# Performance work log

Hardware: AMD Instinct MI355X
Metric: run time of the kernel (lower is better)

The kernel has to match this reference:

```python
import jax, jax.numpy as jnp
import numpy as np
from math import sqrt

EMBED_DIM = 1024
PROJ_DIM = 128
BATCH = 4
SEQ = 4096


def setup_inputs() -> dict:
    key = jax.random.key(0)
    ks = jax.random.split(key, 7)
    x = jax.random.normal(ks[0], (BATCH, SEQ, EMBED_DIM), dtype=jnp.float32)
    # nn.Linear default init scale ~ 1/sqrt(fan_in); use small random weights
    s_e = 1.0 / sqrt(EMBED_DIM)
    Wq = jax.random.uniform(ks[1], (EMBED_DIM, PROJ_DIM), jnp.float32, -s_e, s_e)
    bq = jax.random.uniform(ks[2], (PROJ_DIM,), jnp.float32, -s_e, s_e)
    Wk = jax.random.uniform(ks[3], (EMBED_DIM, PROJ_DIM), jnp.float32, -s_e, s_e)
    bk = jax.random.uniform(ks[4], (PROJ_DIM,), jnp.float32, -s_e, s_e)
    Wov = jax.random.uniform(ks[5], (EMBED_DIM, EMBED_DIM), jnp.float32, -s_e, s_e)
    bov = jax.random.uniform(ks[6], (EMBED_DIM,), jnp.float32, -s_e, s_e)
    return {"x": x, "Wq": Wq, "bq": bq, "Wk": Wk, "bk": bk, "Wov": Wov, "bov": bov}


def reference(x, Wq, bq, Wk, bk, Wov, bov):
    # q, k: (b, s, p); ov: (b, s, d)
    queries = jnp.einsum('bse,ep->bsp', x, Wq) + bq
    keys = jnp.einsum('bse,ep->bsp', x, Wk) + bk
    scores = jnp.einsum('bqp,bkp->bqk', queries, keys) / sqrt(PROJ_DIM)
    pattern = jax.nn.softmax(scores, axis=-1)
    ov = jnp.einsum('bse,ed->bsd', x, Wov) + bov
    return jnp.einsum('bqk,bkd->bqd', pattern, ov)
```

## Files before the change

kernel.cpp:

```cpp
#include <hip/hip_runtime.h>
#include <hip/hip_bf16.h>

#define BATCH 4
#define SEQ   4096
#define EMB   1024
#define PDIM  128

using short8   = __attribute__((ext_vector_type(8))) short;
using ushort8  = __attribute__((ext_vector_type(8))) unsigned short;
using float4v  = __attribute__((ext_vector_type(4))) float;

__device__ __forceinline__ unsigned short f2bf(float f) {
  union { float f; unsigned int u; } x; x.f = f;
  unsigned int r = x.u + 0x7fffu + ((x.u >> 16) & 1u);
  return (unsigned short)(r >> 16);
}

__device__ __forceinline__ void gld_lds16(const unsigned short* g, unsigned short* l) {
  __builtin_amdgcn_global_load_lds(
      (__attribute__((address_space(1))) void*)(g),
      (__attribute__((address_space(3))) void*)(l), 16, 0, 0);
}

__global__ void xprep_kernel(const float* __restrict__ src,
                             unsigned short* __restrict__ rm,
                             unsigned short* __restrict__ tp, int R, int C) {
  __shared__ float tile[32][33];
  const float* s = src + (size_t)blockIdx.z * R * C;
  unsigned short* drm = rm + (size_t)blockIdx.z * R * C;
  unsigned short* dtp = tp + (size_t)blockIdx.z * R * C;
  int c0 = blockIdx.x * 32, r0 = blockIdx.y * 32;
#pragma unroll
  for (int i = 0; i < 32; i += 8) {
    float v = s[(size_t)(r0 + threadIdx.y + i) * C + c0 + threadIdx.x];
    tile[threadIdx.y + i][threadIdx.x] = v;
    drm[(size_t)(r0 + threadIdx.y + i) * C + c0 + threadIdx.x] = f2bf(v);
  }
  __syncthreads();
#pragma unroll
  for (int i = 0; i < 32; i += 8)
    dtp[(size_t)(c0 + threadIdx.y + i) * R + r0 + threadIdx.x] =
        f2bf(tile[threadIdx.x][threadIdx.y + i]);
}

__global__ void transpose_cast_kernel(const float* __restrict__ src,
                                      unsigned short* __restrict__ dst, int R, int C) {
  __shared__ float tile[32][33];
  int c0 = blockIdx.x * 32, r0 = blockIdx.y * 32;
#pragma unroll
  for (int i = 0; i < 32; i += 8)
    tile[threadIdx.y + i][threadIdx.x] =
        src[(size_t)(r0 + threadIdx.y + i) * C + c0 + threadIdx.x];
  __syncthreads();
#pragma unroll
  for (int i = 0; i < 32; i += 8)
    dst[(size_t)(c0 + threadIdx.y + i) * R + r0 + threadIdx.x] =
        f2bf(tile[threadIdx.x][threadIdx.y + i]);
}

__global__ void concat_bias_kernel(const float* __restrict__ a,
                                   const float* __restrict__ b,
                                   float* __restrict__ o) {
  int i = threadIdx.x;
  o[i] = (i < PDIM) ? a[i] : b[i - PDIM];
}

template <int NT>
__global__ __launch_bounds__(256, 2) void gemm_kernel(
    const unsigned short* __restrict__ A, int lda, size_t saz,
    const unsigned short* __restrict__ Bt, int ldb, size_t sbz,
    void* __restrict__ Cv, int ldc, size_t scz,
    int K, const float* __restrict__ bias,
    float* __restrict__ lsum, int slz,
    float scale, int mode) {
  constexpr int NW = NT / 32;
  constexpr int BC = NT / 64;
  __shared__ __attribute__((aligned(16))) unsigned short As[128 * 32];
  __shared__ __attribute__((aligned(16))) unsigned short Bs[NT * 32];
  const int tid = threadIdx.x;
  const int wave = tid >> 6, lane = tid & 63;
  const int quad = lane >> 4, l16 = lane & 15;
  const int m0 = blockIdx.x * 128, n0 = blockIdx.y * NT;
  const int z = blockIdx.z;
  const int mq = (wave >> 1) * 64, nq = (wave & 1) * (NT / 2);

  A  += (size_t)z * saz;
  Bt += (size_t)z * sbz;

  const int lr = lane >> 2;
  const int koff = (((lane & 3) ^ ((lane >> 3) & 3)) << 3);
  const unsigned short* Ag[2];
  unsigned short* Al[2];
#pragma unroll
  for (int j = 0; j < 2; j++) {
    int c = wave * 2 + j;
    Ag[j] = A + (size_t)(m0 + c * 16 + lr) * lda + koff;
    Al[j] = As + c * 512;
  }
  const unsigned short* Bg[BC];
  unsigned short* Bl[BC];
#pragma unroll
  for (int j = 0; j < BC; j++) {
    int c = wave * BC + j;
    Bg[j] = Bt + (size_t)(n0 + c * 16 + lr) * ldb + koff;
    Bl[j] = Bs + c * 512;
  }

  float4v zf = {0.f, 0.f, 0.f, 0.f};
  float4v acc[4][NW];
#pragma unroll
  for (int i = 0; i < 4; i++)
#pragma unroll
    for (int j = 0; j < NW; j++) acc[i][j] = zf;

  const int rsw = ((l16 >> 1) & 3);

  for (int k0 = 0; k0 < K; k0 += 32) {
    if (k0) __syncthreads();
#pragma unroll
    for (int j = 0; j < 2; j++) gld_lds16(Ag[j] + k0, Al[j]);
#pragma unroll
    for (int j = 0; j < BC; j++) gld_lds16(Bg[j] + k0, Bl[j]);
    __syncthreads();

    short8 af[4], bfr[NW];
#pragma unroll
    for (int t = 0; t < 4; t++)
      af[t] = *(const short8*)(As + (mq + t * 16 + l16) * 32 + ((quad ^ rsw) << 3));
#pragma unroll
    for (int t = 0; t < NW; t++)
      bfr[t] = *(const short8*)(Bs + (nq + t * 16 + l16) * 32 + ((quad ^ rsw) << 3));
#pragma unroll
    for (int mt = 0; mt < 4; mt++)
#pragma unroll
      for (int nt = 0; nt < NW; nt++)
        acc[mt][nt] = __builtin_amdgcn_mfma_f32_16x16x32_bf16(af[mt], bfr[nt], acc[mt][nt], 0, 0, 0);
  }

  float* Cf = (float*)Cv + (size_t)z * scz;
  unsigned short* Cb = (unsigned short*)Cv + (size_t)z * scz;

  if (mode == 1) {
    float rsum[4][4];
#pragma unroll
    for (int mt = 0; mt < 4; mt++)
#pragma unroll
      for (int r = 0; r < 4; r++) rsum[mt][r] = 0.f;
#pragma unroll
    for (int mt = 0; mt < 4; mt++)
#pragma unroll
      for (int nt = 0; nt < NW; nt++) {
        int gn = n0 + nq + nt * 16 + l16;
#pragma unroll
        for (int r = 0; r < 4; r++) {
          float e = __expf(acc[mt][nt][r] * scale);
          Cb[(size_t)(m0 + mq + mt * 16 + quad * 4 + r) * ldc + gn] = f2bf(e);
          rsum[mt][r] += e;
        }
      }
#pragma unroll
    for (int mt = 0; mt < 4; mt++)
#pragma unroll
      for (int r = 0; r < 4; r++) {
        float s = rsum[mt][r];
#pragma unroll
        for (int o = 1; o < 16; o <<= 1) s += __shfl_xor(s, o);
        rsum[mt][r] = s;
      }
    if (l16 == 0) {
#pragma unroll
      for (int mt = 0; mt < 4; mt++)
#pragma unroll
        for (int r = 0; r < 4; r++)
          atomicAdd(&lsum[(size_t)z * slz + m0 + mq + mt * 16 + quad * 4 + r], rsum[mt][r]);
    }
  } else if (mode == 2) {
    float linv[4][4];
#pragma unroll
    for (int mt = 0; mt < 4; mt++)
#pragma unroll
      for (int r = 0; r < 4; r++)
        linv[mt][r] = 1.f / lsum[(size_t)z * slz + m0 + mq + mt * 16 + quad * 4 + r];
#pragma unroll
    for (int mt = 0; mt < 4; mt++)
#pragma unroll
      for (int nt = 0; nt < NW; nt++) {
        int gn = n0 + nq + nt * 16 + l16;
#pragma unroll
        for (int r = 0; r < 4; r++)
          Cb[(size_t)(m0 + mq + mt * 16 + quad * 4 + r) * ldc + gn] =
              f2bf(acc[mt][nt][r] * linv[mt][r]);
      }
  } else {
#pragma unroll
    for (int mt = 0; mt < 4; mt++)
#pragma unroll
      for (int nt = 0; nt < NW; nt++) {
        int gn = n0 + nq + nt * 16 + l16;
        float bv = bias[gn];
#pragma unroll
        for (int r = 0; r < 4; r++) {
          int gm = m0 + mq + mt * 16 + quad * 4 + r;
          float v = acc[mt][nt][r] + bv;
          if (mode == 0) Cf[(size_t)gm * ldc + gn] = v;
          else           Cb[(size_t)gm * ldc + gn] = f2bf(v);
        }
      }
  }
}

extern "C" void kernel_launch(void* const* d_in, const int* in_sizes, int n_in,
                              void* d_out, int out_size, void* d_ws, size_t ws_size,
                              hipStream_t stream) {
  const float* x   = (const float*)d_in[0];
  const float* Wq  = (const float*)d_in[1];
  const float* bq  = (const float*)d_in[2];
  const float* Wk  = (const float*)d_in[3];
  const float* bk  = (const float*)d_in[4];
  const float* Wov = (const float*)d_in[5];
  const float* bov = (const float*)d_in[6];
  float* out = (float*)d_out;

  char* ws = (char*)d_ws;
  size_t off = 0;
  auto alloc = [&](size_t bytes) {
    char* p = ws + off;
    off += (bytes + 255) & ~(size_t)255;
    return p;
  };
  const int M = BATCH * SEQ;
  unsigned short* x_bf = (unsigned short*)alloc((size_t)M * EMB * 2);
  unsigned short* xT   = (unsigned short*)alloc((size_t)M * EMB * 2);
  unsigned short* WqkT = (unsigned short*)alloc((size_t)2 * PDIM * EMB * 2);
  unsigned short* WovT = (unsigned short*)alloc((size_t)EMB * EMB * 2);
  float*          bqk  = (float*)alloc(2 * PDIM * sizeof(float));
  unsigned short* qk   = (unsigned short*)alloc((size_t)M * 2 * PDIM * 2);
  float*          linv = (float*)alloc((size_t)M * sizeof(float));
  unsigned short* ctx  = (unsigned short*)alloc((size_t)M * EMB * 2);
  const size_t pslot = (size_t)SEQ * SEQ * 2;
  unsigned short* P = (unsigned short*)(ws + off);
  size_t rem = ws_size > off ? ws_size - off : 0;
  int g = (rem >= 4 * pslot) ? 4 : (rem >= 2 * pslot) ? 2 : 1;

  xprep_kernel<<<dim3(EMB / 32, SEQ / 32, BATCH), dim3(32, 8), 0, stream>>>(x, x_bf, xT, SEQ, EMB);
  transpose_cast_kernel<<<dim3(PDIM / 32, EMB / 32), dim3(32, 8), 0, stream>>>(Wq, WqkT, EMB, PDIM);
  transpose_cast_kernel<<<dim3(PDIM / 32, EMB / 32), dim3(32, 8), 0, stream>>>(Wk, WqkT + (size_t)PDIM * EMB, EMB, PDIM);
  transpose_cast_kernel<<<dim3(EMB / 32, EMB / 32), dim3(32, 8), 0, stream>>>(Wov, WovT, EMB, EMB);
  concat_bias_kernel<<<1, 256, 0, stream>>>(bq, bk, bqk);
  hipMemsetAsync(linv, 0, M * sizeof(float), stream);

  gemm_kernel<128><<<dim3(M / 128, 2, 1), 256, 0, stream>>>(
      x_bf, EMB, 0, WqkT, EMB, 0, qk, 2 * PDIM, 0, EMB, bqk, nullptr, 0, 1.f, 3);

  const float qscale = 0.08838834764831845f;
  for (int b0 = 0; b0 < BATCH; b0 += g) {
    int gg = (b0 + g <= BATCH) ? g : (BATCH - b0);
    gemm_kernel<256><<<dim3(SEQ / 128, SEQ / 256, gg), 256, 0, stream>>>(
        qk + (size_t)b0 * SEQ * 2 * PDIM, 2 * PDIM, (size_t)SEQ * 2 * PDIM,
        qk + (size_t)b0 * SEQ * 2 * PDIM + PDIM, 2 * PDIM, (size_t)SEQ * 2 * PDIM,
        P, SEQ, (size_t)SEQ * SEQ,
        PDIM, nullptr, linv + (size_t)b0 * SEQ, SEQ, qscale, 1);
    gemm_kernel<256><<<dim3(SEQ / 128, EMB / 256, gg), 256, 0, stream>>>(
        P, SEQ, (size_t)SEQ * SEQ,
        xT + (size_t)b0 * EMB * SEQ, SEQ, (size_t)EMB * SEQ,
        ctx + (size_t)b0 * SEQ * EMB, EMB, (size_t)SEQ * EMB,
        SEQ, nullptr, linv + (size_t)b0 * SEQ, SEQ, 1.f, 2);
  }

  gemm_kernel<256><<<dim3(M / 128, EMB / 256, 1), 256, 0, stream>>>(
      ctx, EMB, 0, WovT, EMB, 0, out, EMB, 0, EMB, bov, nullptr, 0, 1.f, 0);
}
```

Baseline: 401.5 us.

## Switch GEMM to 32x32x16 MFMA with K=64 tiles and merge prep kernels

The GEMM kernel moves from 16x16x32 to 32x32x16 bf16 MFMA and doubles the LDS K-tile to 64 with a new XOR swizzle, so each barrier covers more MFMA work and fewer LDS fragment reads are needed. The epilogues are rewritten for the 32x32 accumulator layout. The x prep kernel now uses 64x64 tiles with vectorized float4 loads and ushort8 stores. The weight transposes, bias concat and lsum memset are folded into one launch to cut launch overhead. Risks are higher register pressure at launch_bounds(256,2), strided epilogue stores, and LDS bank conflicts in the 65-wide transpose tile.

```diff
diff --git a/kernel.cpp b/kernel.cpp
--- a/kernel.cpp
+++ b/kernel.cpp
@@ -8,7 +8,9 @@
 
 using short8   = __attribute__((ext_vector_type(8))) short;
 using ushort8  = __attribute__((ext_vector_type(8))) unsigned short;
+using ushort4v = __attribute__((ext_vector_type(4))) unsigned short;
 using float4v  = __attribute__((ext_vector_type(4))) float;
+using float16v = __attribute__((ext_vector_type(16))) float;
 
 __device__ __forceinline__ unsigned short f2bf(float f) {
   union { float f; unsigned int u; } x; x.f = f;
@@ -24,45 +26,64 @@
 
 __global__ void xprep_kernel(const float* __restrict__ src,
                              unsigned short* __restrict__ rm,
-                             unsigned short* __restrict__ tp, int R, int C) {
-  __shared__ float tile[32][33];
-  const float* s = src + (size_t)blockIdx.z * R * C;
-  unsigned short* drm = rm + (size_t)blockIdx.z * R * C;
-  unsigned short* dtp = tp + (size_t)blockIdx.z * R * C;
-  int c0 = blockIdx.x * 32, r0 = blockIdx.y * 32;
-#pragma unroll
-  for (int i = 0; i < 32; i += 8) {
-    float v = s[(size_t)(r0 + threadIdx.y + i) * C + c0 + threadIdx.x];
-    tile[threadIdx.y + i][threadIdx.x] = v;
-    drm[(size_t)(r0 + threadIdx.y + i) * C + c0 + threadIdx.x] = f2bf(v);
+                             unsigned short* __restrict__ tp) {
+  __shared__ float tile[64][65];
+  const int tid = threadIdx.x;
+  const int z = blockIdx.z;
+  const float* s = src + (size_t)z * SEQ * EMB;
+  unsigned short* drm = rm + (size_t)z * SEQ * EMB;
+  unsigned short* dtp = tp + (size_t)z * SEQ * EMB;
+  const int e0 = blockIdx.x * 64, s0 = blockIdx.y * 64;
+#pragma unroll
+  for (int i = 0; i < 4; i++) {
+    int idx = tid + i * 256;
+    int sr = idx >> 4, c4 = (idx & 15) * 4;
+    float4v v = *(const float4v*)(s + (size_t)(s0 + sr) * EMB + e0 + c4);
+    ushort4v o;
+    o[0] = f2bf(v[0]); o[1] = f2bf(v[1]); o[2] = f2bf(v[2]); o[3] = f2bf(v[3]);
+    *(ushort4v*)(drm + (size_t)(s0 + sr) * EMB + e0 + c4) = o;
+    tile[sr][c4] = v[0]; tile[sr][c4 + 1] = v[1];
+    tile[sr][c4 + 2] = v[2]; tile[sr][c4 + 3] = v[3];
   }
   __syncthreads();
 #pragma unroll
+  for (int i = 0; i < 2; i++) {
+    int idx = tid + i * 256;
+    int e = idx >> 3, sc = idx & 7;
+    ushort8 o;
+#pragma unroll
+    for (int j = 0; j < 8; j++) o[j] = f2bf(tile[sc * 8 + j][e]);
+    *(ushort8*)(dtp + (size_t)(e0 + e) * SEQ + s0 + sc * 8) = o;
+  }
+}
+
+__global__ void wprep_kernel(const float* __restrict__ Wq, const float* __restrict__ Wk,
+                             const float* __restrict__ Wov,
+                             unsigned short* __restrict__ WqkT, unsigned short* __restrict__ WovT,
+                             const float* __restrict__ bq, const float* __restrict__ bk,
+                             float* __restrict__ bqk, float* __restrict__ lsum) {
+  __shared__ float t[32][33];
+  const int bid = blockIdx.x, tid = threadIdx.x;
+  const int tx = tid & 31, ty = tid >> 5;
+  const float* src; unsigned short* dst; int C, bx, by;
+  if (bid < 128)        { src = Wq;  dst = WqkT;                       C = PDIM; int b = bid;        bx = b & 3;  by = b >> 2; }
+  else if (bid < 256)   { src = Wk;  dst = WqkT + (size_t)PDIM * EMB;  C = PDIM; int b = bid - 128;  bx = b & 3;  by = b >> 2; }
+  else if (bid < 1280)  { src = Wov; dst = WovT;                       C = EMB;  int b = bid - 256;  bx = b & 31; by = b >> 5; }
+  else if (bid == 1280) {
+    if (tid < 2 * PDIM) bqk[tid] = (tid < PDIM) ? bq[tid] : bk[tid - PDIM];
+    return;
+  } else {
+    lsum[(bid - 1281) * 256 + tid] = 0.f;
+    return;
+  }
+  const int c0 = bx * 32, r0 = by * 32;
+#pragma unroll
   for (int i = 0; i < 32; i += 8)
-    dtp[(size_t)(c0 + threadIdx.y + i) * R + r0 + threadIdx.x] =
-        f2bf(tile[threadIdx.x][threadIdx.y + i]);
-}
-
-__global__ void transpose_cast_kernel(const float* __restrict__ src,
-                                      unsigned short* __restrict__ dst, int R, int C) {
-  __shared__ float tile[32][33];
-  int c0 = blockIdx.x * 32, r0 = blockIdx.y * 32;
+    t[ty + i][tx] = src[(size_t)(r0 + ty + i) * C + c0 + tx];
+  __syncthreads();
 #pragma unroll
   for (int i = 0; i < 32; i += 8)
-    tile[threadIdx.y + i][threadIdx.x] =
-        src[(size_t)(r0 + threadIdx.y + i) * C + c0 + threadIdx.x];
-  __syncthreads();
-#pragma unroll
-  for (int i = 0; i < 32; i += 8)
-    dst[(size_t)(c0 + threadIdx.y + i) * R + r0 + threadIdx.x] =
-        f2bf(tile[threadIdx.x][threadIdx.y + i]);
-}
-
-__global__ void concat_bias_kernel(const float* __restrict__ a,
-                                   const float* __restrict__ b,
-                                   float* __restrict__ o) {
-  int i = threadIdx.x;
-  o[i] = (i < PDIM) ? a[i] : b[i - PDIM];
+    dst[(size_t)(c0 + ty + i) * EMB + r0 + tx] = f2bf(t[tx][ty + i]);
 }
 
 template <int NT>
@@ -73,13 +94,12 @@
     int K, const float* __restrict__ bias,
     float* __restrict__ lsum, int slz,
     float scale, int mode) {
-  constexpr int NW = NT / 32;
-  constexpr int BC = NT / 64;
-  __shared__ __attribute__((aligned(16))) unsigned short As[128 * 32];
-  __shared__ __attribute__((aligned(16))) unsigned short Bs[NT * 32];
+  constexpr int NTW = NT / 64;
+  constexpr int BC  = NT / 32;
+  __shared__ __attribute__((aligned(16))) unsigned short As[128 * 64];
+  __shared__ __attribute__((aligned(16))) unsigned short Bs[NT * 64];
   const int tid = threadIdx.x;
   const int wave = tid >> 6, lane = tid & 63;
-  const int quad = lane >> 4, l16 = lane & 15;
   const int m0 = blockIdx.x * 128, n0 = blockIdx.y * NT;
   const int z = blockIdx.z;
   const int mq = (wave >> 1) * 64, nq = (wave & 1) * (NT / 2);
@@ -87,123 +107,119 @@
   A  += (size_t)z * saz;
   Bt += (size_t)z * sbz;
 
-  const int lr = lane >> 2;
-  const int koff = (((lane & 3) ^ ((lane >> 3) & 3)) << 3);
-  const unsigned short* Ag[2];
-  unsigned short* Al[2];
-#pragma unroll
-  for (int j = 0; j < 2; j++) {
-    int c = wave * 2 + j;
-    Ag[j] = A + (size_t)(m0 + c * 16 + lr) * lda + koff;
+  const int sr = lane >> 3, sc = lane & 7;
+  const int kch = (sc ^ sr) * 8;
+  const unsigned short* Ag[4]; unsigned short* Al[4];
+#pragma unroll
+  for (int j = 0; j < 4; j++) {
+    int c = wave * 4 + j;
+    Ag[j] = A + (size_t)(m0 + c * 8 + sr) * lda + kch;
     Al[j] = As + c * 512;
   }
-  const unsigned short* Bg[BC];
-  unsigned short* Bl[BC];
+  const unsigned short* Bg[BC]; unsigned short* Bl[BC];
 #pragma unroll
   for (int j = 0; j < BC; j++) {
     int c = wave * BC + j;
-    Bg[j] = Bt + (size_t)(n0 + c * 16 + lr) * ldb + koff;
+    Bg[j] = Bt + (size_t)(n0 + c * 8 + sr) * ldb + kch;
     Bl[j] = Bs + c * 512;
   }
 
-  float4v zf = {0.f, 0.f, 0.f, 0.f};
-  float4v acc[4][NW];
-#pragma unroll
-  for (int i = 0; i < 4; i++)
-#pragma unroll
-    for (int j = 0; j < NW; j++) acc[i][j] = zf;
-
-  const int rsw = ((l16 >> 1) & 3);
-
-  for (int k0 = 0; k0 < K; k0 += 32) {
+  float16v acc[2][NTW];
+#pragma unroll
+  for (int i = 0; i < 2; i++)
+#pragma unroll
+    for (int j = 0; j < NTW; j++)
+#pragma unroll
+      for (int r = 0; r < 16; r++) acc[i][j][r] = 0.f;
+
+  const int rt = lane & 31;
+  const int h  = lane >> 5;
+  const int s7 = lane & 7;
+
+  for (int k0 = 0; k0 < K; k0 += 64) {
     if (k0) __syncthreads();
 #pragma unroll
-    for (int j = 0; j < 2; j++) gld_lds16(Ag[j] + k0, Al[j]);
+    for (int j = 0; j < 4; j++) gld_lds16(Ag[j] + k0, Al[j]);
 #pragma unroll
     for (int j = 0; j < BC; j++) gld_lds16(Bg[j] + k0, Bl[j]);
     __syncthreads();
-
-    short8 af[4], bfr[NW];
-#pragma unroll
-    for (int t = 0; t < 4; t++)
-      af[t] = *(const short8*)(As + (mq + t * 16 + l16) * 32 + ((quad ^ rsw) << 3));
-#pragma unroll
-    for (int t = 0; t < NW; t++)
-      bfr[t] = *(const short8*)(Bs + (nq + t * 16 + l16) * 32 + ((quad ^ rsw) << 3));
-#pragma unroll
-    for (int mt = 0; mt < 4; mt++)
-#pragma unroll
-      for (int nt = 0; nt < NW; nt++)
-        acc[mt][nt] = __builtin_amdgcn_mfma_f32_16x16x32_bf16(af[mt], bfr[nt], acc[mt][nt], 0, 0, 0);
-  }
-
-  float* Cf = (float*)Cv + (size_t)z * scz;
-  unsigned short* Cb = (unsigned short*)Cv + (size_t)z * scz;
+#pragma unroll
+    for (int kt = 0; kt < 4; kt++) {
+      const int sl = ((kt * 2 + h) ^ s7) * 8;
+      short8 af[2], bfr[NTW];
+#pragma unroll
+      for (int mt = 0; mt < 2; mt++)
+        af[mt] = *(const short8*)(As + (mq + mt * 32 + rt) * 64 + sl);
+#pragma unroll
+      for (int nt = 0; nt < NTW; nt++)
+        bfr[nt] = *(const short8*)(Bs + (nq + nt * 32 + rt) * 64 + sl);
+#pragma unroll
+      for (int mt = 0; mt < 2; mt++)
+#pragma unroll
+        for (int nt = 0; nt < NTW; nt++)
+          acc[mt][nt] = __builtin_amdgcn_mfma_f32_32x32x16_bf16(af[mt], bfr[nt], acc[mt][nt], 0, 0, 0);
+    }
+  }
 
   if (mode == 1) {
-    float rsum[4][4];
-#pragma unroll
-    for (int mt = 0; mt < 4; mt++)
-#pragma unroll
-      for (int r = 0; r < 4; r++) rsum[mt][r] = 0.f;
-#pragma unroll
-    for (int mt = 0; mt < 4; mt++)
-#pragma unroll
-      for (int nt = 0; nt < NW; nt++) {
-        int gn = n0 + nq + nt * 16 + l16;
-#pragma unroll
-        for (int r = 0; r < 4; r++) {
+    unsigned short* Cb = (unsigned short*)Cv + (size_t)z * scz;
+    float* ls = lsum + (size_t)z * slz;
+#pragma unroll
+    for (int mt = 0; mt < 2; mt++) {
+      float rs[16];
+#pragma unroll
+      for (int r = 0; r < 16; r++) rs[r] = 0.f;
+#pragma unroll
+      for (int r = 0; r < 16; r++) {
+        int gm = m0 + mq + mt * 32 + (r & 3) + 8 * (r >> 2) + 4 * h;
+#pragma unroll
+        for (int nt = 0; nt < NTW; nt++) {
           float e = __expf(acc[mt][nt][r] * scale);
-          Cb[(size_t)(m0 + mq + mt * 16 + quad * 4 + r) * ldc + gn] = f2bf(e);
-          rsum[mt][r] += e;
+          Cb[(size_t)gm * ldc + n0 + nq + nt * 32 + rt] = f2bf(e);
+          rs[r] += e;
         }
       }
 #pragma unroll
-    for (int mt = 0; mt < 4; mt++)
-#pragma unroll
-      for (int r = 0; r < 4; r++) {
-        float s = rsum[mt][r];
-#pragma unroll
-        for (int o = 1; o < 16; o <<= 1) s += __shfl_xor(s, o);
-        rsum[mt][r] = s;
-      }
-    if (l16 == 0) {
-#pragma unroll
-      for (int mt = 0; mt < 4; mt++)
-#pragma unroll
-        for (int r = 0; r < 4; r++)
-          atomicAdd(&lsum[(size_t)z * slz + m0 + mq + mt * 16 + quad * 4 + r], rsum[mt][r]);
+      for (int r = 0; r < 16; r++) {
+        float s = rs[r];
+#pragma unroll
+        for (int o = 1; o < 32; o <<= 1) s += __shfl_xor(s, o);
+        rs[r] = s;
+      }
+      if (rt == 0)
+#pragma unroll
+        for (int r = 0; r < 16; r++)
+          atomicAdd(&ls[m0 + mq + mt * 32 + (r & 3) + 8 * (r >> 2) + 4 * h], rs[r]);
     }
   } else if (mode == 2) {
-    float linv[4][4];
-#pragma unroll
-    for (int mt = 0; mt < 4; mt++)
-#pragma unroll
-      for (int r = 0; r < 4; r++)
-        linv[mt][r] = 1.f / lsum[(size_t)z * slz + m0 + mq + mt * 16 + quad * 4 + r];
-#pragma unroll
-    for (int mt = 0; mt < 4; mt++)
-#pragma unroll
-      for (int nt = 0; nt < NW; nt++) {
-        int gn = n0 + nq + nt * 16 + l16;
-#pragma unroll
-        for (int r = 0; r < 4; r++)
-          Cb[(size_t)(m0 + mq + mt * 16 + quad * 4 + r) * ldc + gn] =
-              f2bf(acc[mt][nt][r] * linv[mt][r]);
+    unsigned short* Cb = (unsigned short*)Cv + (size_t)z * scz;
+    const float* ls = lsum + (size_t)z * slz;
+#pragma unroll
+    for (int mt = 0; mt < 2; mt++)
+#pragma unroll
+      for (int r = 0; r < 16; r++) {
+        int gm = m0 + mq + mt * 32 + (r & 3) + 8 * (r >> 2) + 4 * h;
+        float li = 1.f / ls[gm];
+#pragma unroll
+        for (int nt = 0; nt < NTW; nt++)
+          Cb[(size_t)gm * ldc + n0 + nq + nt * 32 + rt] = f2bf(acc[mt][nt][r] * li);
       }
   } else {
-#pragma unroll
-    for (int mt = 0; mt < 4; mt++)
-#pragma unroll
-      for (int nt = 0; nt < NW; nt++) {
-        int gn = n0 + nq + nt * 16 + l16;
-        float bv = bias[gn];
-#pragma unroll
-        for (int r = 0; r < 4; r++) {
-          int gm = m0 + mq + mt * 16 + quad * 4 + r;
-          float v = acc[mt][nt][r] + bv;
-          if (mode == 0) Cf[(size_t)gm * ldc + gn] = v;
-          else           Cb[(size_t)gm * ldc + gn] = f2bf(v);
+    float* Cf = (float*)Cv + (size_t)z * scz;
+    unsigned short* Cb = (unsigned short*)Cv + (size_t)z * scz;
+    float bv[NTW];
+#pragma unroll
+    for (int nt = 0; nt < NTW; nt++) bv[nt] = bias[n0 + nq + nt * 32 + rt];
+#pragma unroll
+    for (int mt = 0; mt < 2; mt++)
+#pragma unroll
+      for (int r = 0; r < 16; r++) {
+        int gm = m0 + mq + mt * 32 + (r & 3) + 8 * (r >> 2) + 4 * h;
+#pragma unroll
+        for (int nt = 0; nt < NTW; nt++) {
+          float v = acc[mt][nt][r] + bv[nt];
+          if (mode == 0) Cf[(size_t)gm * ldc + n0 + nq + nt * 32 + rt] = v;
+          else           Cb[(size_t)gm * ldc + n0 + nq + nt * 32 + rt] = f2bf(v);
         }
       }
   }
@@ -242,12 +258,8 @@
   size_t rem = ws_size > off ? ws_size - off : 0;
   int g = (rem >= 4 * pslot) ? 4 : (rem >= 2 * pslot) ? 2 : 1;
 
-  xprep_kernel<<<dim3(EMB / 32, SEQ / 32, BATCH), dim3(32, 8), 0, stream>>>(x, x_bf, xT, SEQ, EMB);
-  transpose_cast_kernel<<<dim3(PDIM / 32, EMB / 32), dim3(32, 8), 0, stream>>>(Wq, WqkT, EMB, PDIM);
-  transpose_cast_kernel<<<dim3(PDIM / 32, EMB / 32), dim3(32, 8), 0, stream>>>(Wk, WqkT + (size_t)PDIM * EMB, EMB, PDIM);
-  transpose_cast_kernel<<<dim3(EMB / 32, EMB / 32), dim3(32, 8), 0, stream>>>(Wov, WovT, EMB, EMB);
-  concat_bias_kernel<<<1, 256, 0, stream>>>(bq, bk, bqk);
-  hipMemsetAsync(linv, 0, M * sizeof(float), stream);
+  xprep_kernel<<<dim3(EMB / 64, SEQ / 64, BATCH), 256, 0, stream>>>(x, x_bf, xT);
+  wprep_kernel<<<dim3(1345), 256, 0, stream>>>(Wq, Wk, Wov, WqkT, WovT, bq, bk, bqk, linv);
 
   gemm_kernel<128><<<dim3(M / 128, 2, 1), 256, 0, stream>>>(
       x_bf, EMB, 0, WqkT, EMB, 0, qk, 2 * PDIM, 0, EMB, bqk, nullptr, 0, 1.f, 3);
```

After: 386.8 us. 3.7% less time.
